# Optimization experiments

Hardware: AMD Instinct MI355X
Metric: run time of the kernel (lower is better)

## Reference

```python
import math
import jax, jax.numpy as jnp
import numpy as np

# ---- module hyperparams (from init_kwargs defaults) ----
NUM_AA, EMB_DIM, K, EXCLUDE = 20, 16, 64, 2
R_ON, R_CUT, DELTA, WALL = 8.0, 10.0, 0.3, 10.0
RHO_MIN, RHO_MAX, RHO_BASE = 1.6, 2.8, 2.0
B, L = 8, 2048
BIG = 1e9  # masks excluded pairs in the distance matrix


def setup_inputs() -> dict:
    key = jax.random.key(0)
    k1, k2, k3 = jax.random.split(key, 3)
    # coordinates scaled to a realistic Angstrom spread so switch/softplus are exercised
    R = jax.random.normal(k1, (B, L, 3), dtype=jnp.float32) * 10.0
    seq = jax.random.randint(k2, (B, L), 0, NUM_AA, dtype=jnp.int64)
    # learned params: AA embedding table + size head (small random weight, bias at rho_base)
    emb_table = jax.random.normal(k3, (NUM_AA, EMB_DIM), dtype=jnp.float32)
    size_w = 0.1 * jax.random.normal(jax.random.fold_in(key, 7), (1, EMB_DIM), dtype=jnp.float32)
    frac = (RHO_BASE - RHO_MIN) / max(1e-6, RHO_MAX - RHO_MIN)
    frac = min(0.999, max(0.001, frac))
    size_b = jnp.full((1,), math.log(frac / (1.0 - frac)), dtype=jnp.float32)
    return {"R": R, "seq": seq, "emb_table": emb_table, "size_w": size_w, "size_b": size_b}


def _rho(s, emb_table, size_w, size_b):
    # per-residue learned radius in [RHO_MIN, RHO_MAX]; s: int indices, any shape
    e = emb_table[s]                                  # (..., EMB_DIM)
    x = jnp.einsum('...d,d->...', e, size_w[0]) + size_b[0]
    return RHO_MIN + (RHO_MAX - RHO_MIN) * jax.nn.sigmoid(x)


def _smooth_switch(r):
    # smoothstep from 1 (r<=R_ON) down to 0 (r>=R_CUT)
    t = jnp.clip((r - R_ON) / (R_CUT - R_ON), 0.0, 1.0)
    return 1.0 - t * t * (3.0 - 2.0 * t)


def reference(R, seq, emb_table, size_w, size_b):
    b, l, _ = R.shape
    # pairwise distances (B, L, L)
    diff = R[:, :, None, :] - R[:, None, :, :]
    D = jnp.sqrt(jnp.maximum(jnp.sum(diff * diff, axis=-1), 1e-12))
    # exclude bonded/near-diagonal pairs |i-j| <= EXCLUDE (includes self)
    idx = jnp.arange(l)
    excl = jnp.abs(idx[:, None] - idx[None, :]) <= EXCLUDE
    Dm = jnp.where(excl[None], BIG, D)
    # K smallest distances per residue -> negate for lax.top_k
    neg_r, j = jax.lax.top_k(-Dm, K)                  # (B, L, K)
    r = -neg_r
    # gather neighbor sequence ids along L
    seq_j = jnp.take_along_axis(jnp.broadcast_to(seq[:, :, None], (b, l, K)), j, axis=1)
    # pair radius r0_ij = rho(s_i) + rho(s_j)
    rho_i = _rho(seq, emb_table, size_w, size_b)[:, :, None]   # (B, L, 1)
    rho_j = _rho(seq_j, emb_table, size_w, size_b)             # (B, L, K)
    r0 = rho_i + rho_j
    rep = WALL * jax.nn.softplus((r0 - r) / (DELTA + 1e-12))
    return (rep * _smooth_switch(r)).sum(axis=(1, 2))          # (B,)
```

## Files before the change

kernel.cpp:

```cpp
#include <hip/hip_runtime.h>
#include <hip/hip_fp16.h>
#include <math.h>

#define LRES 2048
#define NB 8
#define KSEL 64
#define EMBD 16
#define NBIN 128
#define BINSCALE 1.28f
#define BINW 0.78125f
#define NSLOT 16

__global__ void prep_kernel(const float* __restrict__ R,
                            const int* __restrict__ seq,
                            const float* __restrict__ emb,
                            const float* __restrict__ w,
                            const float* __restrict__ bias,
                            uint2* __restrict__ pts) {
    int idx = blockIdx.x * blockDim.x + threadIdx.x;
    if (idx < NB * LRES) {
        int s = seq[idx];
        float x = bias[0];
#pragma unroll
        for (int d = 0; d < EMBD; ++d) x += emb[s * EMBD + d] * w[d];
        float rho = 1.6f + 1.2f / (1.0f + expf(-x));
        __half2 h0 = __floats2half2_rn(R[idx * 3 + 0], R[idx * 3 + 1]);
        __half2 h1 = __floats2half2_rn(R[idx * 3 + 2], rho);
        pts[idx] = make_uint2(*(unsigned*)&h0, *(unsigned*)&h1);
    }
}

#define LDS_FENCE() asm volatile("s_waitcnt lgkmcnt(0)" ::: "memory")

__global__ __launch_bounds__(256) void repel_kernel(const uint2* __restrict__ pts,
                                                    float* __restrict__ partial) {
    const int w    = threadIdx.x >> 6;
    const int lane = threadIdx.x & 63;
    const int row  = blockIdx.x * 4 + w;
    const int b    = row >> 11;
    const int i    = row & 2047;

    __shared__ unsigned hist[4][NBIN];
    __shared__ unsigned slots[4][NSLOT][64];
    __shared__ unsigned shT[4];

    const uint2* __restrict__ P = pts + (b << 11);
    const uint4* __restrict__ P4 = (const uint4*)P;

    *(uint2*)&hist[w][lane << 1] = make_uint2(0u, 0u);
    if (lane == 0) shT[w] = NBIN - 1;

    float2 cc0 = __half22float2(*(__half2*)&P[i].x);
    float2 cc1 = __half22float2(*(__half2*)&P[i].y);
    const float cx = cc0.x, cy = cc0.y, cz = cc1.x, rho_i = cc1.y;
    LDS_FENCE();

    unsigned d2u[32];
#pragma unroll
    for (int t = 0; t < 16; ++t) {
        uint4 u = P4[(t << 6) + lane];
        int j0 = (t << 7) + (lane << 1);
        {
            float2 f0 = __half22float2(*(__half2*)&u.x);
            float2 f1 = __half22float2(*(__half2*)&u.y);
            float dx = f0.x - cx, dy = f0.y - cy, dz = f1.x - cz;
            float d2 = dx * dx + dy * dy + dz * dz;
            int dij = j0 - i; dij = (dij < 0) ? -dij : dij;
            unsigned du = (dij <= 2) ? 0xFFFFFFFFu : __float_as_uint(d2);
            d2u[2 * t] = du;
            if (du <= 0x42C7FFFFu)
                atomicAdd(&hist[w][(unsigned)(d2 * BINSCALE)], 1u);
        }
        {
            float2 f0 = __half22float2(*(__half2*)&u.z);
            float2 f1 = __half22float2(*(__half2*)&u.w);
            float dx = f0.x - cx, dy = f0.y - cy, dz = f1.x - cz;
            float d2 = dx * dx + dy * dy + dz * dz;
            int dij = j0 + 1 - i; dij = (dij < 0) ? -dij : dij;
            unsigned du = (dij <= 2) ? 0xFFFFFFFFu : __float_as_uint(d2);
            d2u[2 * t + 1] = du;
            if (du <= 0x42C7FFFFu)
                atomicAdd(&hist[w][(unsigned)(d2 * BINSCALE)], 1u);
        }
    }
    LDS_FENCE();

    uint2 hv = *(const uint2*)&hist[w][lane << 1];
    unsigned p = hv.x + hv.y;
    unsigned s = p;
#pragma unroll
    for (int o = 1; o < 64; o <<= 1) {
        unsigned u = __shfl_up(s, o, 64);
        if (lane >= o) s += u;
    }
    unsigned e0 = s - p;
    if (s >= KSEL && e0 < KSEL) {
        unsigned sub = (e0 + hv.x >= KSEL) ? 0u : 1u;
        shT[w] = (lane << 1) + sub;
    }
    LDS_FENCE();
    const unsigned T = shT[w];
    const unsigned tkb = __float_as_uint((float)(T + 1) * BINW);

    unsigned cnt = 0;
#pragma unroll
    for (int m = 0; m < 32; ++m) {
        if (d2u[m] < tkb && cnt < NSLOT) {
            unsigned j = (unsigned)(((m >> 1) << 7) | (m & 1)) + ((unsigned)lane << 1);
            slots[w][cnt][lane] = (d2u[m] & 0xFFFFF800u) | j;
            ++cnt;
        }
    }
    LDS_FENCE();

    float acc = 0.0f;
    for (unsigned k = 0; k < cnt; ++k) {
        unsigned key = slots[w][k][lane];
        unsigned j = key & 2047u;
        float d2 = __uint_as_float(key & 0xFFFFF800u);
        float r = __fsqrt_rn(fmaxf(d2, 1e-12f));
        uint2 pj = P[j];
        float rho_j = __high2float(*(__half2*)&pj.y);
        float x = (rho_i + rho_j - r) * (1.0f / 0.3f);
        float sp = fmaxf(x, 0.0f) + __logf(1.0f + __expf(-fabsf(x)));
        float t = fminf(fmaxf((r - 8.0f) * 0.5f, 0.0f), 1.0f);
        float sw = 1.0f - t * t * (3.0f - 2.0f * t);
        acc += 10.0f * sp * sw;
    }
#pragma unroll
    for (int o = 32; o > 0; o >>= 1) acc += __shfl_down(acc, o, 64);
    if (lane == 0) partial[row] = acc;
}

__global__ void reduce_kernel(const float* __restrict__ partial, float* __restrict__ out) {
    __shared__ float sh[4];
    const int b = blockIdx.x;
    const int tid = threadIdx.x;
    float acc = 0.0f;
#pragma unroll
    for (int k = 0; k < 8; ++k) acc += partial[(b << 11) + (k << 8) + tid];
#pragma unroll
    for (int o = 32; o > 0; o >>= 1) acc += __shfl_down(acc, o, 64);
    if ((tid & 63) == 0) sh[tid >> 6] = acc;
    __syncthreads();
    if (tid == 0) out[b] = sh[0] + sh[1] + sh[2] + sh[3];
}

extern "C" void kernel_launch(void* const* d_in, const int* in_sizes, int n_in,
                              void* d_out, int out_size, void* d_ws, size_t ws_size,
                              hipStream_t stream) {
    const float* R    = (const float*)d_in[0];
    const int*   seq  = (const int*)d_in[1];
    const float* emb  = (const float*)d_in[2];
    const float* w    = (const float*)d_in[3];
    const float* bias = (const float*)d_in[4];
    float* out = (float*)d_out;

    uint2* pts     = (uint2*)d_ws;
    float* partial = (float*)((char*)d_ws + NB * LRES * sizeof(uint2));

    prep_kernel<<<(NB * LRES + 255) / 256, 256, 0, stream>>>(R, seq, emb, w, bias, pts);
    repel_kernel<<<NB * LRES / 4, 256, 0, stream>>>(pts, partial);
    reduce_kernel<<<NB, 256, 0, stream>>>(partial, out);
}
```

Baseline: 89.82 us.

## Fuse prep and reduce into repel kernel, read fp32 coordinates directly

Drops the prep kernel that packed half-precision coordinates and radii. The main kernel now reads fp32 xyz with float4 loads and computes rho from the embedding on the fly for row i and for each selected neighbour. The reduce kernel is replaced by a block-level sum plus an atomicAdd into the output, cleared first by a memset. Launch overhead and the intermediate buffer go away, but each row reads twice as many bytes, recomputes rho per neighbour, and the atomic summation order is nondeterministic.

```diff
diff --git a/kernel.cpp b/kernel.cpp
--- a/kernel.cpp
+++ b/kernel.cpp
@@ -1,5 +1,4 @@
 #include <hip/hip_runtime.h>
-#include <hip/hip_fp16.h>
 #include <math.h>
 
 #define LRES 2048
@@ -11,74 +10,80 @@
 #define BINW 0.78125f
 #define NSLOT 16
 
-__global__ void prep_kernel(const float* __restrict__ R,
-                            const int* __restrict__ seq,
-                            const float* __restrict__ emb,
-                            const float* __restrict__ w,
-                            const float* __restrict__ bias,
-                            uint2* __restrict__ pts) {
-    int idx = blockIdx.x * blockDim.x + threadIdx.x;
-    if (idx < NB * LRES) {
-        int s = seq[idx];
-        float x = bias[0];
-#pragma unroll
-        for (int d = 0; d < EMBD; ++d) x += emb[s * EMBD + d] * w[d];
-        float rho = 1.6f + 1.2f / (1.0f + expf(-x));
-        __half2 h0 = __floats2half2_rn(R[idx * 3 + 0], R[idx * 3 + 1]);
-        __half2 h1 = __floats2half2_rn(R[idx * 3 + 2], rho);
-        pts[idx] = make_uint2(*(unsigned*)&h0, *(unsigned*)&h1);
-    }
-}
-
 #define LDS_FENCE() asm volatile("s_waitcnt lgkmcnt(0)" ::: "memory")
 
-__global__ __launch_bounds__(256) void repel_kernel(const uint2* __restrict__ pts,
-                                                    float* __restrict__ partial) {
+__global__ __launch_bounds__(256) void repel_kernel(
+    const float* __restrict__ R,
+    const int* __restrict__ seq,
+    const float* __restrict__ emb,
+    const float* __restrict__ wv,
+    const float* __restrict__ bias,
+    float* __restrict__ out)
+{
     const int w    = threadIdx.x >> 6;
     const int lane = threadIdx.x & 63;
     const int row  = blockIdx.x * 4 + w;
     const int b    = row >> 11;
-    const int i    = row & 2047;
+    const int i    = row & (LRES - 1);
 
     __shared__ unsigned hist[4][NBIN];
     __shared__ unsigned slots[4][NSLOT][64];
     __shared__ unsigned shT[4];
+    __shared__ float    shS[4];
 
-    const uint2* __restrict__ P = pts + (b << 11);
-    const uint4* __restrict__ P4 = (const uint4*)P;
+    const float*  __restrict__ Rb = R + b * (LRES * 3);
+    const float4* __restrict__ R4 = (const float4*)Rb;
+    const int*    __restrict__ Sb = seq + b * LRES;
 
     *(uint2*)&hist[w][lane << 1] = make_uint2(0u, 0u);
     if (lane == 0) shT[w] = NBIN - 1;
 
-    float2 cc0 = __half22float2(*(__half2*)&P[i].x);
-    float2 cc1 = __half22float2(*(__half2*)&P[i].y);
-    const float cx = cc0.x, cy = cc0.y, cz = cc1.x, rho_i = cc1.y;
+    const float4 w0 = ((const float4*)wv)[0];
+    const float4 w1 = ((const float4*)wv)[1];
+    const float4 w2 = ((const float4*)wv)[2];
+    const float4 w3 = ((const float4*)wv)[3];
+    const float  bias0 = bias[0];
+
+    const float cx = Rb[i * 3 + 0], cy = Rb[i * 3 + 1], cz = Rb[i * 3 + 2];
+
+    float rho_i;
+    {
+        const float4* e4 = (const float4*)(emb + Sb[i] * EMBD);
+        float4 e0 = e4[0], e1 = e4[1], e2 = e4[2], e3 = e4[3];
+        float x = bias0;
+        x += e0.x * w0.x + e0.y * w0.y + e0.z * w0.z + e0.w * w0.w;
+        x += e1.x * w1.x + e1.y * w1.y + e1.z * w1.z + e1.w * w1.w;
+        x += e2.x * w2.x + e2.y * w2.y + e2.z * w2.z + e2.w * w2.w;
+        x += e3.x * w3.x + e3.y * w3.y + e3.z * w3.z + e3.w * w3.w;
+        rho_i = 1.6f + 1.2f / (1.0f + __expf(-x));
+    }
+
+    const int tlo = ((i - 2 > 0) ? (i - 2) : 0) >> 8;
+    const int thi = ((i + 2 < LRES - 1) ? (i + 2) : (LRES - 1)) >> 8;
+
     LDS_FENCE();
 
     unsigned d2u[32];
 #pragma unroll
-    for (int t = 0; t < 16; ++t) {
-        uint4 u = P4[(t << 6) + lane];
-        int j0 = (t << 7) + (lane << 1);
-        {
-            float2 f0 = __half22float2(*(__half2*)&u.x);
-            float2 f1 = __half22float2(*(__half2*)&u.y);
-            float dx = f0.x - cx, dy = f0.y - cy, dz = f1.x - cz;
+    for (int t = 0; t < 8; ++t) {
+        float4 u0 = R4[t * 192 + lane * 3 + 0];
+        float4 u1 = R4[t * 192 + lane * 3 + 1];
+        float4 u2 = R4[t * 192 + lane * 3 + 2];
+        const int  jb = (t << 8) + (lane << 2);
+        const bool ex = (t == tlo) || (t == thi);
+        float px[4] = {u0.x, u0.w, u1.z, u2.y};
+        float py[4] = {u0.y, u1.x, u1.w, u2.z};
+        float pz[4] = {u0.z, u1.y, u2.x, u2.w};
+#pragma unroll
+        for (int q = 0; q < 4; ++q) {
+            float dx = px[q] - cx, dy = py[q] - cy, dz = pz[q] - cz;
             float d2 = dx * dx + dy * dy + dz * dz;
-            int dij = j0 - i; dij = (dij < 0) ? -dij : dij;
-            unsigned du = (dij <= 2) ? 0xFFFFFFFFu : __float_as_uint(d2);
-            d2u[2 * t] = du;
-            if (du <= 0x42C7FFFFu)
-                atomicAdd(&hist[w][(unsigned)(d2 * BINSCALE)], 1u);
-        }
-        {
-            float2 f0 = __half22float2(*(__half2*)&u.z);
-            float2 f1 = __half22float2(*(__half2*)&u.w);
-            float dx = f0.x - cx, dy = f0.y - cy, dz = f1.x - cz;
-            float d2 = dx * dx + dy * dy + dz * dz;
-            int dij = j0 + 1 - i; dij = (dij < 0) ? -dij : dij;
-            unsigned du = (dij <= 2) ? 0xFFFFFFFFu : __float_as_uint(d2);
-            d2u[2 * t + 1] = du;
+            unsigned du = __float_as_uint(d2);
+            if (ex) {
+                int dij = jb + q - i; dij = (dij < 0) ? -dij : dij;
+                if (dij <= 2) du = 0xFFFFFFFFu;
+            }
+            d2u[t * 4 + q] = du;
             if (du <= 0x42C7FFFFu)
                 atomicAdd(&hist[w][(unsigned)(d2 * BINSCALE)], 1u);
         }
@@ -90,23 +95,23 @@
     unsigned s = p;
 #pragma unroll
     for (int o = 1; o < 64; o <<= 1) {
-        unsigned u = __shfl_up(s, o, 64);
-        if (lane >= o) s += u;
+        unsigned uu = __shfl_up(s, o, 64);
+        if (lane >= o) s += uu;
     }
-    unsigned e0 = s - p;
-    if (s >= KSEL && e0 < KSEL) {
-        unsigned sub = (e0 + hv.x >= KSEL) ? 0u : 1u;
+    unsigned e0s = s - p;
+    if (s >= KSEL && e0s < KSEL) {
+        unsigned sub = (e0s + hv.x >= KSEL) ? 0u : 1u;
         shT[w] = (lane << 1) + sub;
     }
     LDS_FENCE();
-    const unsigned T = shT[w];
+    const unsigned T   = shT[w];
     const unsigned tkb = __float_as_uint((float)(T + 1) * BINW);
 
     unsigned cnt = 0;
 #pragma unroll
     for (int m = 0; m < 32; ++m) {
         if (d2u[m] < tkb && cnt < NSLOT) {
-            unsigned j = (unsigned)(((m >> 1) << 7) | (m & 1)) + ((unsigned)lane << 1);
+            unsigned j = (unsigned)(((m >> 2) << 8) + (m & 3)) + ((unsigned)lane << 2);
             slots[w][cnt][lane] = (d2u[m] & 0xFFFFF800u) | j;
             ++cnt;
         }
@@ -116,34 +121,30 @@
     float acc = 0.0f;
     for (unsigned k = 0; k < cnt; ++k) {
         unsigned key = slots[w][k][lane];
-        unsigned j = key & 2047u;
+        unsigned j   = key & 2047u;
         float d2 = __uint_as_float(key & 0xFFFFF800u);
-        float r = __fsqrt_rn(fmaxf(d2, 1e-12f));
-        uint2 pj = P[j];
-        float rho_j = __high2float(*(__half2*)&pj.y);
-        float x = (rho_i + rho_j - r) * (1.0f / 0.3f);
-        float sp = fmaxf(x, 0.0f) + __logf(1.0f + __expf(-fabsf(x)));
-        float t = fminf(fmaxf((r - 8.0f) * 0.5f, 0.0f), 1.0f);
-        float sw = 1.0f - t * t * (3.0f - 2.0f * t);
+        float r  = __fsqrt_rn(fmaxf(d2, 1e-12f));
+        const float4* e4 = (const float4*)(emb + Sb[j] * EMBD);
+        float4 e0 = e4[0], e1 = e4[1], e2 = e4[2], e3 = e4[3];
+        float x = bias0;
+        x += e0.x * w0.x + e0.y * w0.y + e0.z * w0.z + e0.w * w0.w;
+        x += e1.x * w1.x + e1.y * w1.y + e1.z * w1.z + e1.w * w1.w;
+        x += e2.x * w2.x + e2.y * w2.y + e2.z * w2.z + e2.w * w2.w;
+        x += e3.x * w3.x + e3.y * w3.y + e3.z * w3.z + e3.w * w3.w;
+        float rho_j = 1.6f + 1.2f / (1.0f + __expf(-x));
+        float xx = (rho_i + rho_j - r) * (1.0f / 0.3f);
+        float sp = fmaxf(xx, 0.0f) + __logf(1.0f + __expf(-fabsf(xx)));
+        float tt = fminf(fmaxf((r - 8.0f) * 0.5f, 0.0f), 1.0f);
+        float sw = 1.0f - tt * tt * (3.0f - 2.0f * tt);
         acc += 10.0f * sp * sw;
     }
+
 #pragma unroll
     for (int o = 32; o > 0; o >>= 1) acc += __shfl_down(acc, o, 64);
-    if (lane == 0) partial[row] = acc;
-}
-
-__global__ void reduce_kernel(const float* __restrict__ partial, float* __restrict__ out) {
-    __shared__ float sh[4];
-    const int b = blockIdx.x;
-    const int tid = threadIdx.x;
-    float acc = 0.0f;
-#pragma unroll
-    for (int k = 0; k < 8; ++k) acc += partial[(b << 11) + (k << 8) + tid];
-#pragma unroll
-    for (int o = 32; o > 0; o >>= 1) acc += __shfl_down(acc, o, 64);
-    if ((tid & 63) == 0) sh[tid >> 6] = acc;
+    if (lane == 0) shS[w] = acc;
     __syncthreads();
-    if (tid == 0) out[b] = sh[0] + sh[1] + sh[2] + sh[3];
+    if (threadIdx.x == 0)
+        atomicAdd(&out[b], shS[0] + shS[1] + shS[2] + shS[3]);
 }
 
 extern "C" void kernel_launch(void* const* d_in, const int* in_sizes, int n_in,
@@ -156,10 +157,6 @@
     const float* bias = (const float*)d_in[4];
     float* out = (float*)d_out;
 
-    uint2* pts     = (uint2*)d_ws;
-    float* partial = (float*)((char*)d_ws + NB * LRES * sizeof(uint2));
-
-    prep_kernel<<<(NB * LRES + 255) / 256, 256, 0, stream>>>(R, seq, emb, w, bias, pts);
-    repel_kernel<<<NB * LRES / 4, 256, 0, stream>>>(pts, partial);
-    reduce_kernel<<<NB, 256, 0, stream>>>(partial, out);
+    hipMemsetAsync(out, 0, NB * sizeof(float), stream);
+    repel_kernel<<<NB * LRES / 4, 256, 0, stream>>>(R, seq, emb, w, bias, out);
 }
```

Result: slower. 122.7 us (+36.6%).
